# Kernel tuning notes

Hardware: AMD Instinct MI355X
Metric: run time of the kernel (lower is better)

## Reference

```python
import jax, jax.numpy as jnp
import numpy as np

N_SRC = 100000   # source nodes
N_DST = 50000    # destination nodes
E = 600000       # edges (avg dst degree ~12)
D_IN = 128
D_OUT = 128


def setup_inputs() -> dict:
    key = jax.random.key(0)
    k1, k2, k3, k4 = jax.random.split(key, 4)
    H_src = jax.random.normal(k1, (N_SRC, D_IN), dtype=jnp.float32)
    edge_src = jax.random.randint(k2, (E,), 0, N_SRC)
    edge_dst = jax.random.randint(k3, (E,), 0, N_DST)
    # xavier_uniform-style scale for W
    limit = float(np.sqrt(6.0 / (D_IN + D_OUT)))
    W = jax.random.uniform(k4, (D_IN, D_OUT), dtype=jnp.float32, minval=-limit, maxval=limit)
    b = jnp.zeros((D_OUT,), dtype=jnp.float32)
    return {"H_src": H_src, "W": W, "b": b,
            "edge_src": edge_src, "edge_dst": edge_dst, "n_dst": N_DST}


def reference(H_src, W, b, edge_src, edge_dst, n_dst):
    # Linear transform: WH = H_src @ W + b        [N_src, D_OUT]
    WH = H_src @ W + b
    # Sparse aggregation: (A @ WH) as gather + segment_sum over edges
    agg = jax.ops.segment_sum(WH[edge_src], edge_dst, num_segments=n_dst)  # [N_dst, D_OUT]
    # Degree normalization: deg = row-sum of A, clamped to >= 1
    deg = jax.ops.segment_sum(jnp.ones(edge_dst.shape, WH.dtype), edge_dst,
                              num_segments=n_dst)
    deg = jnp.maximum(deg, 1.0)[:, None]
    return jax.nn.relu(agg / deg)
```

## Files before the change

### kernel.cpp

```cpp
#include <hip/hip_runtime.h>

#define D 128
#define LDA 136
#define BCAP 64
#define CSTRIDE 16
#define OVCAP 65536

typedef __attribute__((ext_vector_type(8))) short bf16x8;
typedef __attribute__((ext_vector_type(4))) float f32x4;
typedef __attribute__((ext_vector_type(4))) unsigned int u32x4;

static __device__ __forceinline__ unsigned short f2bf(float f) {
    unsigned u = __float_as_uint(f);
    unsigned r = 0x7fffu + ((u >> 16) & 1u);
    return (unsigned short)((u + r) >> 16);
}
static __device__ __forceinline__ float bflo(unsigned u) { return __uint_as_float(u << 16); }
static __device__ __forceinline__ float bfhi(unsigned u) { return __uint_as_float(u & 0xffff0000u); }

__global__ __launch_bounds__(256) void zero_wt_kernel(
    const float* __restrict__ W, unsigned short* __restrict__ Wt,
    int* __restrict__ counts, int nz4)
{
    int i = blockIdx.x * 256 + threadIdx.x;
    if (i < nz4) ((u32x4*)counts)[i] = (u32x4){0u, 0u, 0u, 0u};
    if (i < 8192) {
        int n = i >> 6, k2 = (i & 63) << 1;
        unsigned lo = f2bf(W[(size_t)k2 * 128 + n]);
        unsigned hi = f2bf(W[(size_t)(k2 + 1) * 128 + n]);
        ((unsigned*)Wt)[(size_t)n * 64 + (k2 >> 1)] = lo | (hi << 16);
    }
}

__global__ __launch_bounds__(256, 4) void prep_gemm_kernel(
    const float* __restrict__ H, int n_src,
    const unsigned short* __restrict__ Wt, unsigned short* __restrict__ WHb,
    const int* __restrict__ esrc, const int* __restrict__ edst, int E,
    int* __restrict__ counts, int* __restrict__ buckets,
    int* __restrict__ ovcnt, int* __restrict__ ovd, int* __restrict__ ovs)
{
    __shared__ __align__(16) unsigned char smem[34816];
    unsigned short* Wsh = (unsigned short*)smem;
    float* Csh = (float*)smem;

    const int tid = threadIdx.x, bid = blockIdx.x;
    const int gt = (int)gridDim.x * 256;

    int e0 = bid * 256 + tid, e1 = e0 + gt;
    bool h0 = (e0 < E), h1 = (e1 < E);
    int d0 = 0, s0 = 0, d1 = 0, s1 = 0, c0 = 0, c1 = 0;
    if (h0) { d0 = __builtin_nontemporal_load(edst + e0);
              s0 = __builtin_nontemporal_load(esrc + e0); }
    if (h1) { d1 = __builtin_nontemporal_load(edst + e1);
              s1 = __builtin_nontemporal_load(esrc + e1); }
    if (h0) c0 = atomicAdd(&counts[(size_t)d0 * CSTRIDE], 1);
    if (h1) c1 = atomicAdd(&counts[(size_t)d1 * CSTRIDE], 1);

#pragma unroll
    for (int t = 0; t < 8; ++t) {
        int i = tid + t * 256;
        int n = i >> 4, k8 = (i & 15) << 3;
        *(uint4*)&Wsh[n * LDA + k8] = ((const uint4*)Wt)[i];
    }
    __syncthreads();

    const int lane = tid & 63, wvid = tid >> 6;
    const int fl = lane & 15, quad = lane >> 4;
    const int rowbase = bid * 64;
    const bool doG = (rowbase < n_src);

    f32x4 cacc[8];
#pragma unroll
    for (int n = 0; n < 8; ++n) cacc[n] = (f32x4){0.f, 0.f, 0.f, 0.f};

    if (doG) {
        int arow = rowbase + wvid * 16 + fl;
        bool rok = (arow < n_src);
        const f32x4* H4 = (const f32x4*)H;
        size_t base = (size_t)arow * 32 + quad * 2;
        f32x4 z = (f32x4){0.f, 0.f, 0.f, 0.f};
        f32x4 av0 = rok ? H4[base +  0] : z, av1 = rok ? H4[base +  1] : z;
        f32x4 av2 = rok ? H4[base +  8] : z, av3 = rok ? H4[base +  9] : z;
        f32x4 av4 = rok ? H4[base + 16] : z, av5 = rok ? H4[base + 17] : z;
        f32x4 av6 = rok ? H4[base + 24] : z, av7 = rok ? H4[base + 25] : z;

#define PACK_A(a, v0, v1)                                                    \
        { a[0] = (short)f2bf(v0.x); a[1] = (short)f2bf(v0.y);                \
          a[2] = (short)f2bf(v0.z); a[3] = (short)f2bf(v0.w);                \
          a[4] = (short)f2bf(v1.x); a[5] = (short)f2bf(v1.y);                \
          a[6] = (short)f2bf(v1.z); a[7] = (short)f2bf(v1.w); }
#define MSTEP(a, KC)                                                          \
        _Pragma("unroll")                                                     \
        for (int n = 0; n < 8; ++n) {                                         \
            bf16x8 bf = *(const bf16x8*)&Wsh[(n * 16 + fl) * LDA + (KC) + quad * 8]; \
            cacc[n] = __builtin_amdgcn_mfma_f32_16x16x32_bf16(a, bf, cacc[n], 0, 0, 0); \
        }
        bf16x8 a0, a1, a2, a3;
        PACK_A(a0, av0, av1) PACK_A(a1, av2, av3)
        PACK_A(a2, av4, av5) PACK_A(a3, av6, av7)
        MSTEP(a0, 0) MSTEP(a1, 32) MSTEP(a2, 64) MSTEP(a3, 96)
#undef PACK_A
#undef MSTEP
    }
    __syncthreads();

    if (doG) {
#pragma unroll
        for (int n = 0; n < 8; ++n) {
            int col = n * 16 + fl;
#pragma unroll
            for (int r = 0; r < 4; ++r)
                Csh[(wvid * 16 + quad * 4 + r) * 132 + col] = cacc[n][r];
        }
    }
    __syncthreads();

    if (doG) {
#pragma unroll
        for (int t = 0; t < 4; ++t) {
            int i = tid + t * 256;
            int rr = i >> 4, cu = i & 15;
            size_t gr = (size_t)rowbase + rr;
            if (gr < (size_t)n_src) {
                float* s = &Csh[rr * 132 + cu * 8];
                f32x4 lo = *(f32x4*)s, hi = *(f32x4*)(s + 4);
                u32x4 o;
                o.x = (unsigned)f2bf(lo.x) | ((unsigned)f2bf(lo.y) << 16);
                o.y = (unsigned)f2bf(lo.z) | ((unsigned)f2bf(lo.w) << 16);
                o.z = (unsigned)f2bf(hi.x) | ((unsigned)f2bf(hi.y) << 16);
                o.w = (unsigned)f2bf(hi.z) | ((unsigned)f2bf(hi.w) << 16);
                ((u32x4*)WHb)[gr * 16 + cu] = o;
            }
        }
    }

    if (h0) {
        if (c0 < BCAP) buckets[(size_t)d0 * BCAP + c0] = s0;
        else { int o = atomicAdd(ovcnt, 1); if (o < OVCAP) { ovd[o] = d0; ovs[o] = s0; } }
    }
    if (h1) {
        if (c1 < BCAP) buckets[(size_t)d1 * BCAP + c1] = s1;
        else { int o = atomicAdd(ovcnt, 1); if (o < OVCAP) { ovd[o] = d1; ovs[o] = s1; } }
    }
    for (int e = e0 + 2 * gt; e < E; e += gt) {
        int dd = edst[e], ss = esrc[e];
        int cc = atomicAdd(&counts[(size_t)dd * CSTRIDE], 1);
        if (cc < BCAP) buckets[(size_t)dd * BCAP + cc] = ss;
        else { int o = atomicAdd(ovcnt, 1); if (o < OVCAP) { ovd[o] = dd; ovs[o] = ss; } }
    }
}

__global__ __launch_bounds__(256) void agg_finalize_kernel(
    const uint4* __restrict__ WHb, const int* __restrict__ buckets,
    const int* __restrict__ counts, const int* __restrict__ ovcnt,
    const int* __restrict__ ovd, const int* __restrict__ ovs,
    const float* __restrict__ b, float* __restrict__ out, int n_dst)
{
    int dst = blockIdx.x * 4 + (threadIdx.x >> 6);
    if (dst >= n_dst) return;
    int lane = threadIdx.x & 63;
    int dg = counts[(size_t)dst * CSTRIDE];
    int m = dg < BCAP ? dg : BCAP;
    int nov = *ovcnt; if (nov > OVCAP) nov = OVCAP;
    int idx = (lane < m) ? buckets[(size_t)dst * BCAP + lane] : 0;

    const int ql = lane & 15, quad = lane >> 4;
    float acc[8] = {0, 0, 0, 0, 0, 0, 0, 0};
    int j = 0;
    for (; j + 8 <= m; j += 8) {
        int sA = __shfl(idx, j + quad);
        int sB = __shfl(idx, j + 4 + quad);
        uint4 ha = WHb[(size_t)sA * 16 + ql];
        uint4 hb = WHb[(size_t)sB * 16 + ql];
        acc[0] += bflo(ha.x) + bflo(hb.x); acc[1] += bfhi(ha.x) + bfhi(hb.x);
        acc[2] += bflo(ha.y) + bflo(hb.y); acc[3] += bfhi(ha.y) + bfhi(hb.y);
        acc[4] += bflo(ha.z) + bflo(hb.z); acc[5] += bfhi(ha.z) + bfhi(hb.z);
        acc[6] += bflo(ha.w) + bflo(hb.w); acc[7] += bfhi(ha.w) + bfhi(hb.w);
    }
    for (; j < m; j += 4) {
        int jj = j + quad;
        int s = __shfl(idx, jj < m ? jj : m - 1);
        uint4 hv = WHb[(size_t)s * 16 + ql];
        float w = (jj < m) ? 1.f : 0.f;
        acc[0] += w * bflo(hv.x); acc[1] += w * bfhi(hv.x);
        acc[2] += w * bflo(hv.y); acc[3] += w * bfhi(hv.y);
        acc[4] += w * bflo(hv.z); acc[5] += w * bfhi(hv.z);
        acc[6] += w * bflo(hv.w); acc[7] += w * bfhi(hv.w);
    }
    for (int k = quad; k < nov; k += 4) {
        if (ovd[k] == dst) {
            uint4 hv = WHb[(size_t)ovs[k] * 16 + ql];
            acc[0] += bflo(hv.x); acc[1] += bfhi(hv.x);
            acc[2] += bflo(hv.y); acc[3] += bfhi(hv.y);
            acc[4] += bflo(hv.z); acc[5] += bfhi(hv.z);
            acc[6] += bflo(hv.w); acc[7] += bfhi(hv.w);
        }
    }
#pragma unroll
    for (int k = 0; k < 8; ++k) {
        acc[k] += __shfl_xor(acc[k], 16);
        acc[k] += __shfl_xor(acc[k], 32);
    }
    if (quad == 0) {
        float inv  = 1.0f / (float)(dg > 1 ? dg : 1);
        float gate = (dg > 0) ? 1.0f : 0.0f;
        const f32x4* b4 = (const f32x4*)b;
        f32x4 b0 = b4[ql * 2], b1 = b4[ql * 2 + 1];
        f32x4 o0, o1;
        o0.x = fmaxf(acc[0] * inv + b0.x * gate, 0.f);
        o0.y = fmaxf(acc[1] * inv + b0.y * gate, 0.f);
        o0.z = fmaxf(acc[2] * inv + b0.z * gate, 0.f);
        o0.w = fmaxf(acc[3] * inv + b0.w * gate, 0.f);
        o1.x = fmaxf(acc[4] * inv + b1.x * gate, 0.f);
        o1.y = fmaxf(acc[5] * inv + b1.y * gate, 0.f);
        o1.z = fmaxf(acc[6] * inv + b1.z * gate, 0.f);
        o1.w = fmaxf(acc[7] * inv + b1.w * gate, 0.f);
        f32x4* op = (f32x4*)out + (size_t)dst * 32 + ql * 2;
        __builtin_nontemporal_store(o0, op);
        __builtin_nontemporal_store(o1, op + 1);
    }
}

__global__ __launch_bounds__(256) void prep_fb_kernel(
    const int* __restrict__ esrc, const int* __restrict__ edst, int E,
    int* __restrict__ counts, int* __restrict__ buckets,
    int* __restrict__ ovcnt, int* __restrict__ ovd, int* __restrict__ ovs)
{
    int i = blockIdx.x * 256 + threadIdx.x;
    if (i >= E) return;
    int d = edst[i], s = esrc[i];
    int c = atomicAdd(&counts[(size_t)d * CSTRIDE], 1);
    if (c < BCAP) buckets[(size_t)d * BCAP + c] = s;
    else { int o = atomicAdd(ovcnt, 1); if (o < OVCAP) { ovd[o] = d; ovs[o] = s; } }
}

__global__ __launch_bounds__(256) void aggregate_kernel_f32(
    const float* __restrict__ H,
    const int* __restrict__ buckets, const int* __restrict__ counts,
    const int* __restrict__ ovcnt, const int* __restrict__ ovd,
    const int* __restrict__ ovs, unsigned short* __restrict__ aggb, int n_dst)
{
    int dst = blockIdx.x * 4 + (threadIdx.x >> 6);
    if (dst >= n_dst) return;
    int lane = threadIdx.x & 63;
    int dg = counts[(size_t)dst * CSTRIDE];
    int m = dg < BCAP ? dg : BCAP;
    int nov = *ovcnt; if (nov > OVCAP) nov = OVCAP;
    int idx = (lane < m) ? buckets[(size_t)dst * BCAP + lane] : 0;

    const int hl = lane & 31, half = lane >> 5;
    const float4* H4 = (const float4*)H;
    float acc[4] = {0, 0, 0, 0};
    int j = 0;
    for (; j + 4 <= m; j += 4) {
        int sA = __shfl(idx, j + half);
        int sB = __shfl(idx, j + 2 + half);
        float4 va = H4[(size_t)sA * 32 + hl];
        float4 vb = H4[(size_t)sB * 32 + hl];
        acc[0] += va.x + vb.x; acc[1] += va.y + vb.y;
        acc[2] += va.z + vb.z; acc[3] += va.w + vb.w;
    }
    for (; j < m; j += 2) {
        int jj = j + half;
        int s = __shfl(idx, jj < m ? jj : m - 1);
        float4 v = H4[(size_t)s * 32 + hl];
        float w = (jj < m) ? 1.f : 0.f;
        acc[0] += w * v.x; acc[1] += w * v.y;
        acc[2] += w * v.z; acc[3] += w * v.w;
    }
    for (int k = half; k < nov; k += 2) {
        if (ovd[k] == dst) {
            float4 v = H4[(size_t)ovs[k] * 32 + hl];
            acc[0] += v.x; acc[1] += v.y; acc[2] += v.z; acc[3] += v.w;
        }
    }
#pragma unroll
    for (int k = 0; k < 4; ++k) acc[k] += __shfl_xor(acc[k], 32);
    if (half == 0) {
        uint2 o;
        o.x = (unsigned)f2bf(acc[0]) | ((unsigned)f2bf(acc[1]) << 16);
        o.y = (unsigned)f2bf(acc[2]) | ((unsigned)f2bf(acc[3]) << 16);
        ((uint2*)aggb)[(size_t)dst * 32 + hl] = o;
    }
}

__global__ __launch_bounds__(256) void gemm_finalize_kernel(
    const unsigned short* __restrict__ aggb, const unsigned short* __restrict__ Wt,
    const float* __restrict__ b, const int* __restrict__ counts,
    float* __restrict__ out, int n_dst)
{
    __shared__ __align__(16) unsigned char smem[52224];
    unsigned short* Ash = (unsigned short*)smem;
    unsigned short* Wsh = (unsigned short*)(smem + 64 * LDA * 2);
    float* Csh = (float*)smem;

    const int tid  = threadIdx.x;
    const int lane = tid & 63, wv = tid >> 6;
    const size_t row0 = (size_t)blockIdx.x * 64;

#pragma unroll
    for (int t = 0; t < 4; ++t) {
        int i = tid + t * 256;
        int r = i >> 4, k8 = (i & 15) << 3;
        size_t gr = row0 + r;
        uint4 v = (gr < (size_t)n_dst) ? ((const uint4*)aggb)[gr * 16 + (i & 15)]
                                       : make_uint4(0, 0, 0, 0);
        *(uint4*)&Ash[r * LDA + k8] = v;
    }
#pragma unroll
    for (int t = 0; t < 8; ++t) {
        int i = tid + t * 256;
        int n = i >> 4, k8 = (i & 15) << 3;
        *(uint4*)&Wsh[n * LDA + k8] = ((const uint4*)Wt)[i];
    }
    __syncthreads();

    const int m0 = wv * 16;
    const int fl = lane & 15, quad = lane >> 4;

    f32x4 cacc[8];
#pragma unroll
    for (int n = 0; n < 8; ++n) cacc[n] = (f32x4){0.f, 0.f, 0.f, 0.f};

#pragma unroll
    for (int kc = 0; kc < 128; kc += 32) {
        bf16x8 a = *(const bf16x8*)&Ash[(m0 + fl) * LDA + kc + quad * 8];
#pragma unroll
        for (int n = 0; n < 8; ++n) {
            bf16x8 bf = *(const bf16x8*)&Wsh[(n * 16 + fl) * LDA + kc + quad * 8];
            cacc[n] = __builtin_amdgcn_mfma_f32_16x16x32_bf16(a, bf, cacc[n], 0, 0, 0);
        }
    }

    float inv[4], gate[4];
#pragma unroll
    for (int r = 0; r < 4; ++r) {
        size_t gr = row0 + m0 + quad * 4 + r;
        int dg = (gr < (size_t)n_dst) ? counts[gr * CSTRIDE] : 0;
        inv[r]  = 1.0f / (float)(dg > 1 ? dg : 1);
        gate[r] = (dg > 0) ? 1.0f : 0.0f;
    }
    __syncthreads();

#pragma unroll
    for (int n = 0; n < 8; ++n) {
        int col = n * 16 + fl;
        float bc = b[col];
#pragma unroll
        for (int r = 0; r < 4; ++r) {
            float v = cacc[n][r] * inv[r] + bc * gate[r];
            Csh[(m0 + quad * 4 + r) * 132 + col] = fmaxf(v, 0.0f);
        }
    }
    __syncthreads();

#pragma unroll
    for (int t = 0; t < 8; ++t) {
        int i = tid + t * 256;
        int rr = i >> 5, c4 = i & 31;
        size_t gr = row0 + rr;
        if (gr < (size_t)n_dst) {
            f32x4 vout = *(f32x4*)&Csh[rr * 132 + c4 * 4];
            __builtin_nontemporal_store(vout, (f32x4*)out + gr * (D / 4) + c4);
        }
    }
}

extern "C" void kernel_launch(void* const* d_in, const int* in_sizes, int n_in,
                              void* d_out, int out_size, void* d_ws, size_t ws_size,
                              hipStream_t stream) {
    const float* H    = (const float*)d_in[0];
    const float* W    = (const float*)d_in[1];
    const float* b    = (const float*)d_in[2];
    const int*   esrc = (const int*)d_in[3];
    const int*   edst = (const int*)d_in[4];
    const int    E     = in_sizes[3];
    const int    n_dst = out_size / D;
    const int    nsrc_elems = in_sizes[0];
    const int    n_src = nsrc_elems / D;

    float* out = (float*)d_out;

    char* p = (char*)d_ws;
    unsigned short* Wt = (unsigned short*)p;  p += 128 * 128 * sizeof(unsigned short);
    int* counts = (int*)p;  p += (size_t)n_dst * CSTRIDE * 4;
    int* ovcnt  = (int*)p;  p += 256;
    int* ovd    = (int*)p;  p += (size_t)OVCAP * 4;
    int* ovs    = (int*)p;  p += (size_t)OVCAP * 4;
    int* buckets= (int*)p;  p += (size_t)n_dst * BCAP * 4;
    size_t agg_off = (((size_t)(p - (char*)d_ws)) + 255) & ~(size_t)255;
    unsigned short* aggb = (unsigned short*)((char*)d_ws + agg_off);
    size_t wh_off = (agg_off + (size_t)n_dst * D * 2 + 255) & ~(size_t)255;
    bool use_wh = (ws_size >= wh_off + (size_t)nsrc_elems * 2);
    unsigned short* WHb = (unsigned short*)((char*)d_ws + wh_off);

    int nz4 = (n_dst * CSTRIDE + 64) / 4;
    int gz = nz4 > 8192 ? nz4 : 8192;
    zero_wt_kernel<<<(gz + 255) / 256, 256, 0, stream>>>(W, Wt, counts, nz4);

    if (use_wh) {
        int G = (n_src + 63) / 64;
        int Ge = (E + 511) / 512;
        if (Ge > G) G = Ge;
        prep_gemm_kernel<<<G, 256, 0, stream>>>(
            H, n_src, Wt, WHb, esrc, edst, E, counts, buckets, ovcnt, ovd, ovs);
        agg_finalize_kernel<<<(n_dst + 3) / 4, 256, 0, stream>>>(
            (const uint4*)WHb, buckets, counts, ovcnt, ovd, ovs, b, out, n_dst);
    } else {
        prep_fb_kernel<<<(E + 255) / 256, 256, 0, stream>>>(
            esrc, edst, E, counts, buckets, ovcnt, ovd, ovs);
        aggregate_kernel_f32<<<(n_dst + 3) / 4, 256, 0, stream>>>(
            H, buckets, counts, ovcnt, ovd, ovs, aggb, n_dst);
        gemm_finalize_kernel<<<(n_dst + 63) / 64, 256, 0, stream>>>(
            aggb, Wt, b, counts, out, n_dst);
    }
}
```

Before: 163.1 us.

## Read W fragments from global, shrink LDS to bf16 staging, drop block barriers

The GEMM phase no longer stages the transposed bf16 W into shared memory. Each wave reads its B fragments straight from global/L2, and the output is converted to bf16 before being staged in a smaller per-wave LDS tile. That tile is then written out by the same wave, so the block-wide __syncthreads are no longer needed. Launch bounds go from 4 to 6 blocks per CU to use the freed LDS for occupancy. The trade-off is more global/cache traffic for W, since every wave re-reads 32KB, and possible register-pressure effects from the higher occupancy target.

```diff
diff --git a/kernel.cpp b/kernel.cpp
--- a/kernel.cpp
+++ b/kernel.cpp
@@ -32,16 +32,14 @@
     }
 }
 
-__global__ __launch_bounds__(256, 4) void prep_gemm_kernel(
+__global__ __launch_bounds__(256, 6) void prep_gemm_kernel(
     const float* __restrict__ H, int n_src,
     const unsigned short* __restrict__ Wt, unsigned short* __restrict__ WHb,
     const int* __restrict__ esrc, const int* __restrict__ edst, int E,
     int* __restrict__ counts, int* __restrict__ buckets,
     int* __restrict__ ovcnt, int* __restrict__ ovd, int* __restrict__ ovs)
 {
-    __shared__ __align__(16) unsigned char smem[34816];
-    unsigned short* Wsh = (unsigned short*)smem;
-    float* Csh = (float*)smem;
+    __shared__ __align__(16) unsigned short Csh[64 * LDA];
 
     const int tid = threadIdx.x, bid = blockIdx.x;
     const int gt = (int)gridDim.x * 256;
@@ -56,25 +54,13 @@
     if (h0) c0 = atomicAdd(&counts[(size_t)d0 * CSTRIDE], 1);
     if (h1) c1 = atomicAdd(&counts[(size_t)d1 * CSTRIDE], 1);
 
-#pragma unroll
-    for (int t = 0; t < 8; ++t) {
-        int i = tid + t * 256;
-        int n = i >> 4, k8 = (i & 15) << 3;
-        *(uint4*)&Wsh[n * LDA + k8] = ((const uint4*)Wt)[i];
-    }
-    __syncthreads();
-
     const int lane = tid & 63, wvid = tid >> 6;
     const int fl = lane & 15, quad = lane >> 4;
     const int rowbase = bid * 64;
-    const bool doG = (rowbase < n_src);
-
-    f32x4 cacc[8];
-#pragma unroll
-    for (int n = 0; n < 8; ++n) cacc[n] = (f32x4){0.f, 0.f, 0.f, 0.f};
-
-    if (doG) {
-        int arow = rowbase + wvid * 16 + fl;
+    const int m0 = wvid * 16;
+
+    if (rowbase < n_src) {
+        int arow = rowbase + m0 + fl;
         bool rok = (arow < n_src);
         const f32x4* H4 = (const f32x4*)H;
         size_t base = (size_t)arow * 32 + quad * 2;
@@ -84,6 +70,10 @@
         f32x4 av4 = rok ? H4[base + 16] : z, av5 = rok ? H4[base + 17] : z;
         f32x4 av6 = rok ? H4[base + 24] : z, av7 = rok ? H4[base + 25] : z;
 
+        f32x4 cacc[8];
+#pragma unroll
+        for (int n = 0; n < 8; ++n) cacc[n] = (f32x4){0.f, 0.f, 0.f, 0.f};
+
 #define PACK_A(a, v0, v1)                                                    \
         { a[0] = (short)f2bf(v0.x); a[1] = (short)f2bf(v0.y);                \
           a[2] = (short)f2bf(v0.z); a[3] = (short)f2bf(v0.w);                \
@@ -92,7 +82,7 @@
 #define MSTEP(a, KC)                                                          \
         _Pragma("unroll")                                                     \
         for (int n = 0; n < 8; ++n) {                                         \
-            bf16x8 bf = *(const bf16x8*)&Wsh[(n * 16 + fl) * LDA + (KC) + quad * 8]; \
+            bf16x8 bf = *(const bf16x8*)&Wt[(n * 16 + fl) * 128 + (KC) + quad * 8]; \
             cacc[n] = __builtin_amdgcn_mfma_f32_16x16x32_bf16(a, bf, cacc[n], 0, 0, 0); \
         }
         bf16x8 a0, a1, a2, a3;
@@ -101,35 +91,22 @@
         MSTEP(a0, 0) MSTEP(a1, 32) MSTEP(a2, 64) MSTEP(a3, 96)
 #undef PACK_A
 #undef MSTEP
-    }
-    __syncthreads();
-
-    if (doG) {
+
 #pragma unroll
         for (int n = 0; n < 8; ++n) {
             int col = n * 16 + fl;
 #pragma unroll
             for (int r = 0; r < 4; ++r)
-                Csh[(wvid * 16 + quad * 4 + r) * 132 + col] = cacc[n][r];
-        }
-    }
-    __syncthreads();
-
-    if (doG) {
+                Csh[(m0 + quad * 4 + r) * LDA + col] = f2bf(cacc[n][r]);
+        }
 #pragma unroll
         for (int t = 0; t < 4; ++t) {
-            int i = tid + t * 256;
-            int rr = i >> 4, cu = i & 15;
-            size_t gr = (size_t)rowbase + rr;
+            int c = lane + t * 64;
+            int row = m0 + (c >> 4), chunk = c & 15;
+            size_t gr = (size_t)rowbase + row;
             if (gr < (size_t)n_src) {
-                float* s = &Csh[rr * 132 + cu * 8];
-                f32x4 lo = *(f32x4*)s, hi = *(f32x4*)(s + 4);
-                u32x4 o;
-                o.x = (unsigned)f2bf(lo.x) | ((unsigned)f2bf(lo.y) << 16);
-                o.y = (unsigned)f2bf(lo.z) | ((unsigned)f2bf(lo.w) << 16);
-                o.z = (unsigned)f2bf(hi.x) | ((unsigned)f2bf(hi.y) << 16);
-                o.w = (unsigned)f2bf(hi.z) | ((unsigned)f2bf(hi.w) << 16);
-                ((u32x4*)WHb)[gr * 16 + cu] = o;
+                u32x4 v = *(const u32x4*)&Csh[row * LDA + chunk * 8];
+                ((u32x4*)WHb)[gr * 16 + chunk] = v;
             }
         }
     }
```

Result: slower. 178.8 us (+9.6%).
